# Performance work log

Measured on AMD Instinct MI355X. Metric: run time of the kernel, lower is better.

The kernel has to match this reference:

```python
import jax, jax.numpy as jnp
import numpy as np

NUM_EXPERTS = 8
IN_F = 1024
OUT_F = 1024
N_TOK = 8192


def setup_inputs() -> dict:
    key = jax.random.key(0)
    ks = jax.random.split(key, 5)
    scale_in = 1.0 / np.sqrt(IN_F)
    x = jax.random.normal(ks[0], (N_TOK, IN_F), dtype=jnp.float32)
    # stacked expert weights [E, in, out] and biases [E, out]
    We = jax.random.uniform(ks[1], (NUM_EXPERTS, IN_F, OUT_F), dtype=jnp.float32, minval=-scale_in, maxval=scale_in)
    be = jax.random.uniform(ks[2], (NUM_EXPERTS, OUT_F), dtype=jnp.float32, minval=-scale_in, maxval=scale_in)
    # gate: Linear(in_features, num_experts)
    Wg = jax.random.uniform(ks[3], (IN_F, NUM_EXPERTS), dtype=jnp.float32, minval=-scale_in, maxval=scale_in)
    bg = jax.random.uniform(ks[4], (NUM_EXPERTS,), dtype=jnp.float32, minval=-scale_in, maxval=scale_in)
    return {"x": x, "We": We, "be": be, "Wg": Wg, "bg": bg}


def reference(x, We, be, Wg, bg):
    # gate_score: softmax over experts  [N, E]
    gate_score = jax.nn.softmax(x @ Wg + bg, axis=-1)
    # all-experts dense outputs  [N, E, out]
    expert_outputs = jnp.einsum('ni,eio->neo', x, We) + be[None, :, :]
    # gate-weighted combine  [N, out]
    return jnp.einsum('ne,neo->no', gate_score, expert_outputs)
```

## Files before the change

### kernel.cpp

```cpp
#include <hip/hip_runtime.h>
#include <hip/hip_bf16.h>

#define M_TOK 8192
#define IN_F  1024
#define OUT_F 1024
#define N_EXP 8
#define KT    8192

typedef __attribute__((ext_vector_type(8))) _Float16 f16x8;
typedef __attribute__((ext_vector_type(4))) _Float16 f16x4;
typedef __attribute__((ext_vector_type(4))) float    f32x4;

__global__ __launch_bounds__(256) void moe_gate_kernel(
    const float* __restrict__ x, const float* __restrict__ Wg,
    const float* __restrict__ bg, float* __restrict__ g, _Float16* __restrict__ xh)
{
    const int lane = threadIdx.x & 63;
    const int wave = threadIdx.x >> 6;
    const int t0 = blockIdx.x * 16 + wave * 4;
    const float* xr0 = x + (size_t)t0 * IN_F;

    float acc[4][8] = {};
#pragma unroll
    for (int kc = 0; kc < 4; ++kc) {
        const int i = kc * 256 + lane * 4;
        float4 xv[4];
#pragma unroll
        for (int tk = 0; tk < 4; ++tk) xv[tk] = *(const float4*)(xr0 + (size_t)tk * IN_F + i);
        float xs[4][4];
#pragma unroll
        for (int tk = 0; tk < 4; ++tk) {
            xs[tk][0] = xv[tk].x; xs[tk][1] = xv[tk].y;
            xs[tk][2] = xv[tk].z; xs[tk][3] = xv[tk].w;
        }
#pragma unroll
        for (int j = 0; j < 4; ++j) {
            const float4* wr = (const float4*)(Wg + (size_t)(i + j) * 8);
            float4 w0 = wr[0], w1 = wr[1];
            float wv[8] = {w0.x, w0.y, w0.z, w0.w, w1.x, w1.y, w1.z, w1.w};
#pragma unroll
            for (int tk = 0; tk < 4; ++tk)
#pragma unroll
                for (int e = 0; e < 8; ++e)
                    acc[tk][e] = fmaf(xs[tk][j], wv[e], acc[tk][e]);
        }
#pragma unroll
        for (int tk = 0; tk < 4; ++tk) {
            f16x4 h = { (_Float16)xs[tk][0], (_Float16)xs[tk][1],
                        (_Float16)xs[tk][2], (_Float16)xs[tk][3] };
            *(f16x4*)(xh + (size_t)(t0 + tk) * IN_F + i) = h;
        }
    }
#pragma unroll
    for (int tk = 0; tk < 4; ++tk) {
        float a[8];
#pragma unroll
        for (int e = 0; e < 8; ++e) {
            float v = acc[tk][e];
#pragma unroll
            for (int off = 32; off > 0; off >>= 1) v += __shfl_xor(v, off, 64);
            a[e] = v + bg[e];
        }
        float mx = a[0];
#pragma unroll
        for (int e = 1; e < 8; ++e) mx = fmaxf(mx, a[e]);
        float sum = 0.f;
#pragma unroll
        for (int e = 0; e < 8; ++e) { a[e] = __expf(a[e] - mx); sum += a[e]; }
        float inv = 1.0f / sum;
        if (lane == 0) {
            float4 p0 = {a[0] * inv, a[1] * inv, a[2] * inv, a[3] * inv};
            float4 p1 = {a[4] * inv, a[5] * inv, a[6] * inv, a[7] * inv};
            float4* gp = (float4*)(g + (size_t)(t0 + tk) * 8);
            gp[0] = p0; gp[1] = p1;
        }
    }
}

__global__ __launch_bounds__(256) void moe_transpose_kernel(
    const float* __restrict__ We, _Float16* __restrict__ wt)
{
    __shared__ float t[64][65];
    const int bid = blockIdx.x;
    const int e  = bid >> 8;
    const int o0 = ((bid >> 4) & 15) * 64;
    const int i0 = (bid & 15) * 64;
    const float* src = We + ((size_t)e << 20);
    const int oo = threadIdx.x & 63;
    const int ib = threadIdx.x >> 6;
#pragma unroll
    for (int r = 0; r < 16; ++r) {
        int i = ib + r * 4;
        t[i][oo] = src[(size_t)(i0 + i) * OUT_F + o0 + oo];
    }
    __syncthreads();
    const int i8 = threadIdx.x & 7;
    const int ob = threadIdx.x >> 3;
#pragma unroll
    for (int h = 0; h < 2; ++h) {
        const int o = ob + h * 32;
        float v[8];
#pragma unroll
        for (int j = 0; j < 8; ++j) v[j] = t[i8 * 8 + j][o];
        f16x8 hv = { (_Float16)v[0], (_Float16)v[1], (_Float16)v[2], (_Float16)v[3],
                     (_Float16)v[4], (_Float16)v[5], (_Float16)v[6], (_Float16)v[7] };
        *(f16x8*)(wt + (size_t)(o0 + o) * KT + (size_t)e * 1024 + i0 + i8 * 8) = hv;
    }
}

__device__ __forceinline__ void async16(const void* gp, void* lp) {
    __builtin_amdgcn_global_load_lds((const __attribute__((address_space(1))) void*)gp,
                                     (__attribute__((address_space(3))) void*)lp, 16, 0, 0);
}

__global__ __launch_bounds__(256, 2) void moe_gemm_kernel(
    const _Float16* __restrict__ xh,
    const _Float16* __restrict__ wt,
    const float* __restrict__ g,
    const float* __restrict__ be,
    float* __restrict__ out)
{
    __shared__ __align__(16) _Float16 As[128 * 64];
    __shared__ __align__(16) _Float16 Bs[128 * 64];
    __shared__ float gs[8 * 128];
    __shared__ float bs[8 * 128];

    const int tid  = threadIdx.x;
    const int lane = tid & 63;
    const int wave = tid >> 6;
    const size_t n0 = (size_t)blockIdx.x * 128;
    const size_t m0 = (size_t)blockIdx.y * 128;

    {
        float4 v = ((const float4*)(g + m0 * 8))[tid];
        int row = tid >> 1, e0 = (tid & 1) * 4;
        gs[(e0 + 0) * 128 + row] = v.x;
        gs[(e0 + 1) * 128 + row] = v.y;
        gs[(e0 + 2) * 128 + row] = v.z;
        gs[(e0 + 3) * 128 + row] = v.w;
    }
#pragma unroll
    for (int r = 0; r < 4; ++r) {
        int idx = r * 256 + tid;
        int eb = idx >> 7, col = idx & 127;
        bs[idx] = be[(size_t)eb * 1024 + n0 + col];
    }
    __syncthreads();

    const int rb = tid >> 3;
    const int c8 = (tid & 7) ^ (rb & 7);
    const _Float16* pA = xh + (m0 + rb) * (size_t)IN_F + c8 * 8;
    const _Float16* pB = wt + (n0 + rb) * (size_t)KT + c8 * 8;
    char* lA = (char*)As + tid * 16;
    char* lB = (char*)Bs + tid * 16;

    const int quad = lane >> 4;
    const int ml   = lane & 15;
    const int wm   = (wave >> 1) * 64;
    const int wn   = (wave & 1) * 64;
    const int raA0 = (wm + ml) * 128 + (((0 * 4 + quad) ^ (lane & 7)) * 16);
    const int raA1 = (wm + ml) * 128 + (((1 * 4 + quad) ^ (lane & 7)) * 16);
    const int raB0 = (wn + ml) * 128 + (((0 * 4 + quad) ^ (lane & 7)) * 16);
    const int raB1 = (wn + ml) * 128 + (((1 * 4 + quad) ^ (lane & 7)) * 16);

    f32x4 acc[4][4] = {};
#pragma unroll
    for (int e = 0; e < 8; ++e) {
        float ge[4][4], bb[4];
#pragma unroll
        for (int i = 0; i < 4; ++i)
#pragma unroll
            for (int r = 0; r < 4; ++r) ge[i][r] = gs[e * 128 + wm + i * 16 + quad * 4 + r];
#pragma unroll
        for (int jn = 0; jn < 4; ++jn) bb[jn] = bs[e * 128 + wn + jn * 16 + ml];
#pragma unroll
        for (int i = 0; i < 4; ++i)
#pragma unroll
            for (int jn = 0; jn < 4; ++jn)
#pragma unroll
                for (int r = 0; r < 4; ++r)
                    acc[i][jn][r] = fmaf(ge[i][r], bb[jn], acc[i][jn][r]);
    }

    _Float16 gh[8][4];
#pragma unroll
    for (int e = 0; e < 8; ++e)
#pragma unroll
        for (int t = 0; t < 4; ++t)
            gh[e][t] = (_Float16)gs[e * 128 + wm + t * 16 + ml];

    for (int kt = 0; kt < 16; ++kt) {
        const _Float16* sA = pA + kt * 64;
#pragma unroll
        for (int j = 0; j < 4; ++j) async16(sA + j * 32 * (size_t)IN_F, lA + j * 4096);

        f16x8 afr[2][4];
#pragma unroll
        for (int e = 0; e < 8; ++e) {
            const _Float16* sB = pB + e * 1024 + kt * 64;
#pragma unroll
            for (int j = 0; j < 4; ++j) async16(sB + j * 32 * (size_t)KT, lB + j * 4096);
            __syncthreads();
            if (e == 0) {
#pragma unroll
                for (int t = 0; t < 4; ++t) {
                    afr[0][t] = *(const f16x8*)((const char*)As + raA0 + t * 2048);
                    afr[1][t] = *(const f16x8*)((const char*)As + raA1 + t * 2048);
                }
            }
#pragma unroll
            for (int s = 0; s < 2; ++s) {
                const int rB = s ? raB1 : raB0;
                f16x8 af[4], bf[4];
#pragma unroll
                for (int t = 0; t < 4; ++t) bf[t] = *(const f16x8*)((const char*)Bs + rB + t * 2048);
#pragma unroll
                for (int t = 0; t < 4; ++t) af[t] = afr[s][t] * gh[e][t];
#pragma unroll
                for (int i = 0; i < 4; ++i)
#pragma unroll
                    for (int jn = 0; jn < 4; ++jn)
                        acc[i][jn] = __builtin_amdgcn_mfma_f32_16x16x32_f16(af[i], bf[jn], acc[i][jn], 0, 0, 0);
            }
            __syncthreads();
        }
    }

#pragma unroll
    for (int i = 0; i < 4; ++i) {
        const int rowb = wm + i * 16 + quad * 4;
#pragma unroll
        for (int jn = 0; jn < 4; ++jn) {
            const size_t col = n0 + wn + jn * 16 + ml;
#pragma unroll
            for (int r = 0; r < 4; ++r)
                out[(m0 + rowb + r) * (size_t)OUT_F + col] = acc[i][jn][r];
        }
    }
}

extern "C" void kernel_launch(void* const* d_in, const int* in_sizes, int n_in,
                              void* d_out, int out_size, void* d_ws, size_t ws_size,
                              hipStream_t stream) {
    const float* x  = (const float*)d_in[0];
    const float* We = (const float*)d_in[1];
    const float* be = (const float*)d_in[2];
    const float* Wg = (const float*)d_in[3];
    const float* bg = (const float*)d_in[4];
    float* out = (float*)d_out;

    char* ws = (char*)d_ws;
    float*    g   = (float*)ws;
    _Float16* xh  = (_Float16*)(ws + (1 << 18));
    _Float16* wt2 = (_Float16*)(ws + (1 << 18) + (1 << 24));

    moe_gate_kernel<<<512, 256, 0, stream>>>(x, Wg, bg, g, xh);
    moe_transpose_kernel<<<2048, 256, 0, stream>>>(We, wt2);
    moe_gemm_kernel<<<dim3(OUT_F / 128, M_TOK / 128), 256, 0, stream>>>(xh, wt2, g, be, out);
}
```

Measured before the change: 242.0 us.

## Fuse gate, weight transpose and GEMM into one persistent kernel with grid barrier

Merges the three kernels into a single 512-block launch. Each block first does its gate/softmax and x-to-fp16 slice, then transposes four weight tiles. A global atomic-counter barrier separates these phases from the GEMM. This removes two kernel launches and their inter-kernel gaps. In exchange it relies on all 512 blocks being co-resident (2 per CU via launch bounds), and the spin barrier has a timeout that could break correctness if residency fails.

```diff
diff --git a/kernel.cpp b/kernel.cpp
--- a/kernel.cpp
+++ b/kernel.cpp
@@ -11,125 +11,143 @@
 typedef __attribute__((ext_vector_type(4))) _Float16 f16x4;
 typedef __attribute__((ext_vector_type(4))) float    f32x4;
 
-__global__ __launch_bounds__(256) void moe_gate_kernel(
-    const float* __restrict__ x, const float* __restrict__ Wg,
-    const float* __restrict__ bg, float* __restrict__ g, _Float16* __restrict__ xh)
-{
-    const int lane = threadIdx.x & 63;
-    const int wave = threadIdx.x >> 6;
-    const int t0 = blockIdx.x * 16 + wave * 4;
-    const float* xr0 = x + (size_t)t0 * IN_F;
-
-    float acc[4][8] = {};
-#pragma unroll
-    for (int kc = 0; kc < 4; ++kc) {
-        const int i = kc * 256 + lane * 4;
-        float4 xv[4];
-#pragma unroll
-        for (int tk = 0; tk < 4; ++tk) xv[tk] = *(const float4*)(xr0 + (size_t)tk * IN_F + i);
-        float xs[4][4];
-#pragma unroll
-        for (int tk = 0; tk < 4; ++tk) {
-            xs[tk][0] = xv[tk].x; xs[tk][1] = xv[tk].y;
-            xs[tk][2] = xv[tk].z; xs[tk][3] = xv[tk].w;
-        }
-#pragma unroll
-        for (int j = 0; j < 4; ++j) {
-            const float4* wr = (const float4*)(Wg + (size_t)(i + j) * 8);
-            float4 w0 = wr[0], w1 = wr[1];
-            float wv[8] = {w0.x, w0.y, w0.z, w0.w, w1.x, w1.y, w1.z, w1.w};
-#pragma unroll
-            for (int tk = 0; tk < 4; ++tk)
-#pragma unroll
-                for (int e = 0; e < 8; ++e)
-                    acc[tk][e] = fmaf(xs[tk][j], wv[e], acc[tk][e]);
-        }
-#pragma unroll
-        for (int tk = 0; tk < 4; ++tk) {
-            f16x4 h = { (_Float16)xs[tk][0], (_Float16)xs[tk][1],
-                        (_Float16)xs[tk][2], (_Float16)xs[tk][3] };
-            *(f16x4*)(xh + (size_t)(t0 + tk) * IN_F + i) = h;
-        }
-    }
-#pragma unroll
-    for (int tk = 0; tk < 4; ++tk) {
-        float a[8];
-#pragma unroll
-        for (int e = 0; e < 8; ++e) {
-            float v = acc[tk][e];
-#pragma unroll
-            for (int off = 32; off > 0; off >>= 1) v += __shfl_xor(v, off, 64);
-            a[e] = v + bg[e];
-        }
-        float mx = a[0];
-#pragma unroll
-        for (int e = 1; e < 8; ++e) mx = fmaxf(mx, a[e]);
-        float sum = 0.f;
-#pragma unroll
-        for (int e = 0; e < 8; ++e) { a[e] = __expf(a[e] - mx); sum += a[e]; }
-        float inv = 1.0f / sum;
-        if (lane == 0) {
-            float4 p0 = {a[0] * inv, a[1] * inv, a[2] * inv, a[3] * inv};
-            float4 p1 = {a[4] * inv, a[5] * inv, a[6] * inv, a[7] * inv};
-            float4* gp = (float4*)(g + (size_t)(t0 + tk) * 8);
-            gp[0] = p0; gp[1] = p1;
-        }
-    }
-}
-
-__global__ __launch_bounds__(256) void moe_transpose_kernel(
-    const float* __restrict__ We, _Float16* __restrict__ wt)
-{
-    __shared__ float t[64][65];
-    const int bid = blockIdx.x;
-    const int e  = bid >> 8;
-    const int o0 = ((bid >> 4) & 15) * 64;
-    const int i0 = (bid & 15) * 64;
-    const float* src = We + ((size_t)e << 20);
-    const int oo = threadIdx.x & 63;
-    const int ib = threadIdx.x >> 6;
-#pragma unroll
-    for (int r = 0; r < 16; ++r) {
-        int i = ib + r * 4;
-        t[i][oo] = src[(size_t)(i0 + i) * OUT_F + o0 + oo];
-    }
-    __syncthreads();
-    const int i8 = threadIdx.x & 7;
-    const int ob = threadIdx.x >> 3;
-#pragma unroll
-    for (int h = 0; h < 2; ++h) {
-        const int o = ob + h * 32;
-        float v[8];
-#pragma unroll
-        for (int j = 0; j < 8; ++j) v[j] = t[i8 * 8 + j][o];
-        f16x8 hv = { (_Float16)v[0], (_Float16)v[1], (_Float16)v[2], (_Float16)v[3],
-                     (_Float16)v[4], (_Float16)v[5], (_Float16)v[6], (_Float16)v[7] };
-        *(f16x8*)(wt + (size_t)(o0 + o) * KT + (size_t)e * 1024 + i0 + i8 * 8) = hv;
-    }
-}
+__device__ unsigned long long moe_bar_cnt = 0ull;
 
 __device__ __forceinline__ void async16(const void* gp, void* lp) {
     __builtin_amdgcn_global_load_lds((const __attribute__((address_space(1))) void*)gp,
                                      (__attribute__((address_space(3))) void*)lp, 16, 0, 0);
 }
 
-__global__ __launch_bounds__(256, 2) void moe_gemm_kernel(
-    const _Float16* __restrict__ xh,
-    const _Float16* __restrict__ wt,
-    const float* __restrict__ g,
-    const float* __restrict__ be,
+__global__ __launch_bounds__(256, 2) void moe_fused_kernel(
+    const float* __restrict__ x,   const float* __restrict__ We,
+    const float* __restrict__ be,  const float* __restrict__ Wg,
+    const float* __restrict__ bg,
+    float* __restrict__ g, _Float16* __restrict__ xh, _Float16* __restrict__ wt,
     float* __restrict__ out)
 {
-    __shared__ __align__(16) _Float16 As[128 * 64];
-    __shared__ __align__(16) _Float16 Bs[128 * 64];
-    __shared__ float gs[8 * 128];
-    __shared__ float bs[8 * 128];
+    __shared__ __align__(16) char smem[40960];
 
     const int tid  = threadIdx.x;
     const int lane = tid & 63;
     const int wave = tid >> 6;
-    const size_t n0 = (size_t)blockIdx.x * 128;
-    const size_t m0 = (size_t)blockIdx.y * 128;
+    const int bid  = blockIdx.x;
+
+    {
+        const int t0 = bid * 16 + wave * 4;
+        const float* xr0 = x + (size_t)t0 * IN_F;
+        float acc[4][8] = {};
+#pragma unroll
+        for (int kc = 0; kc < 4; ++kc) {
+            const int i = kc * 256 + lane * 4;
+            float4 xv[4];
+#pragma unroll
+            for (int tk = 0; tk < 4; ++tk) xv[tk] = *(const float4*)(xr0 + (size_t)tk * IN_F + i);
+            float xs[4][4];
+#pragma unroll
+            for (int tk = 0; tk < 4; ++tk) {
+                xs[tk][0] = xv[tk].x; xs[tk][1] = xv[tk].y;
+                xs[tk][2] = xv[tk].z; xs[tk][3] = xv[tk].w;
+            }
+#pragma unroll
+            for (int j = 0; j < 4; ++j) {
+                const float4* wr = (const float4*)(Wg + (size_t)(i + j) * 8);
+                float4 w0 = wr[0], w1 = wr[1];
+                float wv[8] = {w0.x, w0.y, w0.z, w0.w, w1.x, w1.y, w1.z, w1.w};
+#pragma unroll
+                for (int tk = 0; tk < 4; ++tk)
+#pragma unroll
+                    for (int e = 0; e < 8; ++e)
+                        acc[tk][e] = fmaf(xs[tk][j], wv[e], acc[tk][e]);
+            }
+#pragma unroll
+            for (int tk = 0; tk < 4; ++tk) {
+                f16x4 h = { (_Float16)xs[tk][0], (_Float16)xs[tk][1],
+                            (_Float16)xs[tk][2], (_Float16)xs[tk][3] };
+                *(f16x4*)(xh + (size_t)(t0 + tk) * IN_F + i) = h;
+            }
+        }
+#pragma unroll
+        for (int tk = 0; tk < 4; ++tk) {
+            float a[8];
+#pragma unroll
+            for (int e = 0; e < 8; ++e) {
+                float v = acc[tk][e];
+#pragma unroll
+                for (int off = 32; off > 0; off >>= 1) v += __shfl_xor(v, off, 64);
+                a[e] = v + bg[e];
+            }
+            float mx = a[0];
+#pragma unroll
+            for (int e = 1; e < 8; ++e) mx = fmaxf(mx, a[e]);
+            float sum = 0.f;
+#pragma unroll
+            for (int e = 0; e < 8; ++e) { a[e] = __expf(a[e] - mx); sum += a[e]; }
+            float inv = 1.0f / sum;
+            if (lane == 0) {
+                float4 p0 = {a[0] * inv, a[1] * inv, a[2] * inv, a[3] * inv};
+                float4 p1 = {a[4] * inv, a[5] * inv, a[6] * inv, a[7] * inv};
+                float4* gp = (float4*)(g + (size_t)(t0 + tk) * 8);
+                gp[0] = p0; gp[1] = p1;
+            }
+        }
+    }
+
+    {
+        float (*t)[65] = (float (*)[65])smem;
+        const int oo = tid & 63;
+        const int ib = tid >> 6;
+        const int i8 = tid & 7;
+        const int ob = tid >> 3;
+#pragma unroll 1
+        for (int c = 0; c < 4; ++c) {
+            const int tile = bid * 4 + c;
+            const int e  = tile >> 8;
+            const int o0 = ((tile >> 4) & 15) * 64;
+            const int i0 = (tile & 15) * 64;
+            const float* src = We + ((size_t)e << 20);
+            __syncthreads();
+#pragma unroll
+            for (int r = 0; r < 16; ++r) {
+                int i = ib + r * 4;
+                t[i][oo] = src[(size_t)(i0 + i) * OUT_F + o0 + oo];
+            }
+            __syncthreads();
+#pragma unroll
+            for (int h = 0; h < 2; ++h) {
+                const int o = ob + h * 32;
+                float v[8];
+#pragma unroll
+                for (int j = 0; j < 8; ++j) v[j] = t[i8 * 8 + j][o];
+                f16x8 hv = { (_Float16)v[0], (_Float16)v[1], (_Float16)v[2], (_Float16)v[3],
+                             (_Float16)v[4], (_Float16)v[5], (_Float16)v[6], (_Float16)v[7] };
+                *(f16x8*)(wt + (size_t)(o0 + o) * KT + (size_t)e * 1024 + i0 + i8 * 8) = hv;
+            }
+        }
+    }
+
+    __syncthreads();
+    __threadfence();
+    if (tid == 0) {
+        unsigned long long old = __hip_atomic_fetch_add(&moe_bar_cnt, 1ull,
+                                    __ATOMIC_ACQ_REL, __HIP_MEMORY_SCOPE_AGENT);
+        unsigned long long target = (old / 512ull + 1ull) * 512ull;
+        int spins = 0;
+        while (__hip_atomic_load(&moe_bar_cnt, __ATOMIC_ACQUIRE,
+                                 __HIP_MEMORY_SCOPE_AGENT) < target) {
+            __builtin_amdgcn_s_sleep(10);
+            if (++spins > 200000) break;
+        }
+    }
+    __syncthreads();
+    __threadfence();
+
+    _Float16* As = (_Float16*)smem;
+    _Float16* Bs = (_Float16*)(smem + 16384);
+    float*    gs = (float*)(smem + 32768);
+    float*    bsh= (float*)(smem + 36864);
+
+    const size_t n0 = (size_t)(bid & 7) * 128;
+    const size_t m0 = (size_t)(bid >> 3) * 128;
 
     {
         float4 v = ((const float4*)(g + m0 * 8))[tid];
@@ -143,7 +161,7 @@
     for (int r = 0; r < 4; ++r) {
         int idx = r * 256 + tid;
         int eb = idx >> 7, col = idx & 127;
-        bs[idx] = be[(size_t)eb * 1024 + n0 + col];
+        bsh[idx] = be[(size_t)eb * 1024 + n0 + col];
     }
     __syncthreads();
 
@@ -172,7 +190,7 @@
 #pragma unroll
             for (int r = 0; r < 4; ++r) ge[i][r] = gs[e * 128 + wm + i * 16 + quad * 4 + r];
 #pragma unroll
-        for (int jn = 0; jn < 4; ++jn) bb[jn] = bs[e * 128 + wn + jn * 16 + ml];
+        for (int jn = 0; jn < 4; ++jn) bb[jn] = bsh[e * 128 + wn + jn * 16 + ml];
 #pragma unroll
         for (int i = 0; i < 4; ++i)
 #pragma unroll
@@ -254,7 +272,5 @@
     _Float16* xh  = (_Float16*)(ws + (1 << 18));
     _Float16* wt2 = (_Float16*)(ws + (1 << 18) + (1 << 24));
 
-    moe_gate_kernel<<<512, 256, 0, stream>>>(x, Wg, bg, g, xh);
-    moe_transpose_kernel<<<2048, 256, 0, stream>>>(We, wt2);
-    moe_gemm_kernel<<<dim3(OUT_F / 128, M_TOK / 128), 256, 0, stream>>>(xh, wt2, g, be, out);
+    moe_fused_kernel<<<512, 256, 0, stream>>>(x, We, be, Wg, bg, g, xh, wt2, out);
 }
```

Result: slower. 426.9 us (+76.4%).
